# Performance work log

Measured on AMD Instinct MI355X. Metric: run time of the kernel, lower is better.

## Reference

```python
import jax, jax.numpy as jnp
import numpy as np

N = 50000
V_FEATS = 128
FILTERS = 128
K = 20


def setup_inputs() -> dict:
    key = jax.random.key(0)
    ks = jax.random.split(key, 8)
    vertices = jax.random.normal(ks[0], (N, V_FEATS), dtype=jnp.float32)
    nh_indices = jax.random.randint(ks[1], (N, K), 0, N, dtype=jnp.int32)
    int_idx = jax.random.randint(ks[2], (N, K), 0, N, dtype=jnp.int32)
    mask = jax.random.uniform(ks[3], (N, K)) < 0.3
    int_indices = jnp.where(mask, jnp.int32(-1), int_idx)
    nh_edges = jax.random.normal(ks[4], (N, K), dtype=jnp.float32)
    int_edges = jax.random.normal(ks[5], (N, K), dtype=jnp.float32)
    # kaiming-uniform-ish init for params
    bound = float(np.sqrt(6.0 / V_FEATS))
    Wvc = jax.random.uniform(ks[6], (V_FEATS, FILTERS), minval=-bound, maxval=bound, dtype=jnp.float32)
    Wvn = jax.random.uniform(ks[7], (V_FEATS, FILTERS), minval=-bound, maxval=bound, dtype=jnp.float32)
    bv = jnp.zeros((FILTERS,), dtype=jnp.float32)
    return {"vertices": vertices, "nh_indices": nh_indices, "int_indices": int_indices,
            "nh_edges": nh_edges, "int_edges": int_edges, "Wvc": Wvc, "Wvn": Wvn, "bv": bv}


def reference(vertices, nh_indices, int_indices, nh_edges, int_edges, Wvc, Wvn, bv):
    # [N, 2K] concatenated neighbor + interface indices / edge weights
    indices = jnp.concatenate([nh_indices, int_indices], axis=1)
    edges = jnp.concatenate([nh_edges, int_edges], axis=1)[..., None]  # [N,2K,1]
    part = (indices != -1).astype(vertices.dtype)[..., None]           # [N,2K,1] validity mask
    Zc = vertices @ Wvc                                                # [N,F] center term
    v_Wvn = vertices @ Wvn                                             # [N,F]
    gathered = v_Wvn[indices]  # [N,2K,F]; -1 wraps to last row, zeroed by mask (same as torch)
    denom = jnp.sum(indices > -1, axis=1, keepdims=True).astype(vertices.dtype)  # [N,1]
    Zn = jnp.sum(gathered * part * edges, axis=1) / denom             # [N,F]
    z = jax.nn.relu(Zc + Zn + bv)
    return z
```

## Files before the change

### kernel.cpp

```cpp
#include <hip/hip_runtime.h>

#define NV 50000
#define F 128
#define K 20
#define KCAT 256
#define RPB 16

typedef __attribute__((ext_vector_type(8))) __bf16 bf16x8;
typedef __attribute__((ext_vector_type(4))) float f32x4;

__device__ inline ushort f2bf(float x) {
    uint u = __float_as_uint(x);
    return (ushort)((u + 0x7fffu + ((u >> 16) & 1u)) >> 16);
}


__global__ __launch_bounds__(256) void prep_kernel(
    const f32x4* __restrict__ v4, ushort* __restrict__ vb,
    const float* __restrict__ Wvc, const float* __restrict__ Wvn,
    ushort* __restrict__ wt)
{
    int bid = blockIdx.x;
    if (bid < NV * F / 4 / 256) {
        int t = bid * 256 + threadIdx.x;
        int e = t * 4;
        int row = e >> 7, f = e & 127;
        f32x4 x = __builtin_nontemporal_load(v4 + t);
        uint2 o;
        o.x = (uint)f2bf(x[0]) | ((uint)f2bf(x[1]) << 16);
        o.y = (uint)f2bf(x[2]) | ((uint)f2bf(x[3]) << 16);
        *reinterpret_cast<uint2*>(vb + (size_t)row * KCAT + f) = o;
    } else {
        int t = (bid - NV * F / 4 / 256) * 256 + threadIdx.x;
        int c = t >> 8, k = t & 255;
        float w = (k < F) ? Wvc[k * F + c] : Wvn[(k - F) * F + c];
        wt[t] = f2bf(w);
    }
}

__global__ __launch_bounds__(256) void agg_lds(
    const uint* __restrict__ vb_u,
    const int* __restrict__ nh_idx, const int* __restrict__ int_idx,
    const float* __restrict__ nh_e, const float* __restrict__ int_e,
    uint* __restrict__ vagg_u)
{
    __shared__ int2 sJW[RPB][2 * K];
    __shared__ int  sCnt[RPB];

    const int tid = threadIdx.x;
    const int r0  = blockIdx.x * RPB;

    if (tid < RPB) sCnt[tid] = K;
    for (int x = tid; x < RPB * K; x += 256) {
        int r = x / K, k = x - r * K;
        long g = (long)r0 * K + x;
        sJW[r][k] = make_int2(nh_idx[g], __float_as_int(nh_e[g]));
    }
    __syncthreads();
    for (int x = tid; x < RPB * K; x += 256) {
        int r = x / K, k = x - r * K;
        long g = (long)r0 * K + x;
        int   j = int_idx[g];
        float w = int_e[g];
        bool  valid = (j >= 0);
        sJW[r][K + k] = make_int2(valid ? j : 0, valid ? __float_as_int(w) : 0);
        if (valid) atomicAdd(&sCnt[r], 1);
    }
    __syncthreads();

    const int slice = tid >> 6;
    const int lane  = tid & 63;
    const int q     = lane & 15;
    const int rsub  = lane >> 4;
    const uint* __restrict__ src = vb_u + slice * 16 + q;

    #pragma unroll 1
    for (int rq = 0; rq < RPB / 4; ++rq) {
        const int r = rq * 4 + rsub;
        float ax = 0.f, ay = 0.f;
        #pragma unroll 8
        for (int k = 0; k < 2 * K; ++k) {
            int2  jw = sJW[r][k];
            float w  = __int_as_float(jw.y);
            uint  p  = src[(size_t)jw.x * 128];
            ax = fmaf(w, __uint_as_float(p << 16), ax);
            ay = fmaf(w, __uint_as_float(p & 0xffff0000u), ay);
        }
        float inv = 1.f / (float)sCnt[r];
        vagg_u[(size_t)(r0 + r) * 128 + 64 + slice * 16 + q] =
            (uint)f2bf(ax * inv) | ((uint)f2bf(ay * inv) << 16);
    }
}

__global__ __launch_bounds__(256) void gemm_fused(
    const ushort* __restrict__ vb,
    const ushort* __restrict__ wt,
    const float* __restrict__ bv,
    float* __restrict__ out)
{
    const int lane = threadIdx.x & 63;
    const int wave = threadIdx.x >> 6;
    const int r0   = blockIdx.x * 64 + wave * 16;

    int arow = r0 + (lane & 15);
    if (arow >= NV) arow = NV - 1;

    const bf16x8* abase = reinterpret_cast<const bf16x8*>(
        vb + (size_t)arow * KCAT + (lane >> 4) * 8);
    bf16x8 a[8];
    #pragma unroll
    for (int ks = 0; ks < 8; ++ks)
        a[ks] = __builtin_nontemporal_load(abase + ks * 4);

    const ushort* wbase = wt + (size_t)(lane & 15) * KCAT + (lane >> 4) * 8;
    const int col0  = lane & 15;
    const int rbase = r0 + (lane >> 4) * 4;

    #pragma unroll 1
    for (int ct = 0; ct < 8; ++ct) {
        const bf16x8* wb = reinterpret_cast<const bf16x8*>(
            wbase + (size_t)ct * 16 * KCAT);
        f32x4 acc = (f32x4){0.f, 0.f, 0.f, 0.f};
        #pragma unroll
        for (int ks = 0; ks < 8; ++ks) {
            bf16x8 b = wb[ks * 4];
            acc = __builtin_amdgcn_mfma_f32_16x16x32_bf16(a[ks], b, acc, 0, 0, 0);
        }
        int c = ct * 16 + col0;
        float bb = bv[c];
        #pragma unroll
        for (int reg = 0; reg < 4; ++reg) {
            int r = rbase + reg;
            if (r < NV) {
                float z = acc[reg] + bb;
                __builtin_nontemporal_store(fmaxf(z, 0.f), out + (size_t)r * F + c);
            }
        }
    }
}

extern "C" void kernel_launch(void* const* d_in, const int* in_sizes, int n_in,
                              void* d_out, int out_size, void* d_ws, size_t ws_size,
                              hipStream_t stream)
{
    const float* v       = (const float*)d_in[0];
    const int*   nh_idx  = (const int*)  d_in[1];
    const int*   int_idx = (const int*)  d_in[2];
    const float* nh_e    = (const float*)d_in[3];
    const float* int_e   = (const float*)d_in[4];
    const float* Wvc     = (const float*)d_in[5];
    const float* Wvn     = (const float*)d_in[6];
    const float* bv      = (const float*)d_in[7];
    float* out = (float*)d_out;

    ushort* vb = (ushort*)d_ws;
    ushort* wt = vb + (size_t)NV * KCAT;

    prep_kernel<<<NV * F / 4 / 256 + F * KCAT / 256, 256, 0, stream>>>(
        (const f32x4*)v, vb, Wvc, Wvn, wt);
    agg_lds<<<NV / RPB, 256, 0, stream>>>((const uint*)vb, nh_idx, int_idx,
                                          nh_e, int_e, (uint*)vb);
    gemm_fused<<<(NV + 63) / 64, 256, 0, stream>>>(vb, wt, bv, out);
}
```

Measured before the change: 179.4 us.

## Gather neighbor features from an FP8 copy of vertices in aggregation

The prep kernel now also writes an FP8 (e4m3) copy of the vertex features, and the aggregation kernel gathers neighbor rows from it instead of the bf16 copy. This halves the bytes per random gather. The thread mapping also changes: each thread handles one row and 8 features, and loads 8 bytes per neighbor. The goal is less gather bandwidth and fewer load instructions, at the cost of an extra FP8 write in prep and a larger quantization error on the aggregated features.

```diff
diff --git a/kernel.cpp b/kernel.cpp
--- a/kernel.cpp
+++ b/kernel.cpp
@@ -8,6 +8,7 @@
 
 typedef __attribute__((ext_vector_type(8))) __bf16 bf16x8;
 typedef __attribute__((ext_vector_type(4))) float f32x4;
+typedef __attribute__((ext_vector_type(2))) float f32x2;
 
 __device__ inline ushort f2bf(float x) {
     uint u = __float_as_uint(x);
@@ -17,6 +18,7 @@
 
 __global__ __launch_bounds__(256) void prep_kernel(
     const f32x4* __restrict__ v4, ushort* __restrict__ vb,
+    uchar* __restrict__ v8,
     const float* __restrict__ Wvc, const float* __restrict__ Wvn,
     ushort* __restrict__ wt)
 {
@@ -30,6 +32,9 @@
         o.x = (uint)f2bf(x[0]) | ((uint)f2bf(x[1]) << 16);
         o.y = (uint)f2bf(x[2]) | ((uint)f2bf(x[3]) << 16);
         *reinterpret_cast<uint2*>(vb + (size_t)row * KCAT + f) = o;
+        int p8 = __builtin_amdgcn_cvt_pk_fp8_f32(x[0], x[1], 0, false);
+        p8     = __builtin_amdgcn_cvt_pk_fp8_f32(x[2], x[3], p8, true);
+        *reinterpret_cast<uint*>(v8 + (size_t)row * F + f) = (uint)p8;
     } else {
         int t = (bid - NV * F / 4 / 256) * 256 + threadIdx.x;
         int c = t >> 8, k = t & 255;
@@ -38,13 +43,13 @@
     }
 }
 
-__global__ __launch_bounds__(256) void agg_lds(
-    const uint* __restrict__ vb_u,
+__global__ __launch_bounds__(256) void agg_fp8(
+    const uchar* __restrict__ v8,
     const int* __restrict__ nh_idx, const int* __restrict__ int_idx,
     const float* __restrict__ nh_e, const float* __restrict__ int_e,
-    uint* __restrict__ vagg_u)
+    ushort* __restrict__ vb)
 {
-    __shared__ int2 sJW[RPB][2 * K];
+    __shared__ int2 sJW[RPB][2 * K + 1];
     __shared__ int  sCnt[RPB];
 
     const int tid = threadIdx.x;
@@ -70,26 +75,39 @@
 
     const int slice = tid >> 6;
     const int lane  = tid & 63;
-    const int q     = lane & 15;
-    const int rsub  = lane >> 4;
-    const uint* __restrict__ src = vb_u + slice * 16 + q;
+    const int q     = lane & 3;
+    const int r     = lane >> 2;
+    const uchar* __restrict__ src = v8 + slice * 32 + q * 8;
 
-    #pragma unroll 1
-    for (int rq = 0; rq < RPB / 4; ++rq) {
-        const int r = rq * 4 + rsub;
-        float ax = 0.f, ay = 0.f;
-        #pragma unroll 8
-        for (int k = 0; k < 2 * K; ++k) {
-            int2  jw = sJW[r][k];
-            float w  = __int_as_float(jw.y);
-            uint  p  = src[(size_t)jw.x * 128];
-            ax = fmaf(w, __uint_as_float(p << 16), ax);
-            ay = fmaf(w, __uint_as_float(p & 0xffff0000u), ay);
-        }
-        float inv = 1.f / (float)sCnt[r];
-        vagg_u[(size_t)(r0 + r) * 128 + 64 + slice * 16 + q] =
-            (uint)f2bf(ax * inv) | ((uint)f2bf(ay * inv) << 16);
+    float acc[8];
+    #pragma unroll
+    for (int i = 0; i < 8; ++i) acc[i] = 0.f;
+
+    #pragma unroll 4
+    for (int k = 0; k < 2 * K; ++k) {
+        int2  jw = sJW[r][k];
+        float w  = __int_as_float(jw.y);
+        uint2 p  = *reinterpret_cast<const uint2*>(src + (size_t)jw.x * F);
+        f32x2 f01 = __builtin_amdgcn_cvt_pk_f32_fp8(p.x, false);
+        f32x2 f23 = __builtin_amdgcn_cvt_pk_f32_fp8(p.x, true);
+        f32x2 f45 = __builtin_amdgcn_cvt_pk_f32_fp8(p.y, false);
+        f32x2 f67 = __builtin_amdgcn_cvt_pk_f32_fp8(p.y, true);
+        acc[0] = fmaf(w, f01[0], acc[0]);
+        acc[1] = fmaf(w, f01[1], acc[1]);
+        acc[2] = fmaf(w, f23[0], acc[2]);
+        acc[3] = fmaf(w, f23[1], acc[3]);
+        acc[4] = fmaf(w, f45[0], acc[4]);
+        acc[5] = fmaf(w, f45[1], acc[5]);
+        acc[6] = fmaf(w, f67[0], acc[6]);
+        acc[7] = fmaf(w, f67[1], acc[7]);
     }
+    float inv = 1.f / (float)sCnt[r];
+    uint4 o;
+    o.x = (uint)f2bf(acc[0] * inv) | ((uint)f2bf(acc[1] * inv) << 16);
+    o.y = (uint)f2bf(acc[2] * inv) | ((uint)f2bf(acc[3] * inv) << 16);
+    o.z = (uint)f2bf(acc[4] * inv) | ((uint)f2bf(acc[5] * inv) << 16);
+    o.w = (uint)f2bf(acc[6] * inv) | ((uint)f2bf(acc[7] * inv) << 16);
+    *reinterpret_cast<uint4*>(vb + (size_t)(r0 + r) * KCAT + F + slice * 32 + q * 8) = o;
 }
 
 __global__ __launch_bounds__(256) void gemm_fused(
@@ -155,10 +173,10 @@
 
     ushort* vb = (ushort*)d_ws;
     ushort* wt = vb + (size_t)NV * KCAT;
+    uchar*  v8 = (uchar*)(wt + (size_t)F * KCAT);
 
     prep_kernel<<<NV * F / 4 / 256 + F * KCAT / 256, 256, 0, stream>>>(
-        (const f32x4*)v, vb, Wvc, Wvn, wt);
-    agg_lds<<<NV / RPB, 256, 0, stream>>>((const uint*)vb, nh_idx, int_idx,
-                                          nh_e, int_e, (uint*)vb);
+        (const f32x4*)v, vb, v8, Wvc, Wvn, wt);
+    agg_fp8<<<NV / RPB, 256, 0, stream>>>(v8, nh_idx, int_idx, nh_e, int_e, vb);
     gemm_fused<<<(NV + 63) / 64, 256, 0, stream>>>(vb, wt, bv, out);
 }
```

Result: faster. 160.0 us (-10.8%).
